# Kernel optimization log

Hardware: AMD Instinct MI355X
Metric: run time of the kernel (lower is better)

## Reference

```python
import jax, jax.numpy as jnp
import numpy as np
from math import sqrt

B = 16
SEQ = 2048          # tokens per sequence (equal-length jagged layout)
L = B * SEQ         # total tokens
D = 512             # embedding dim
P = 8192            # num_position_buckets
NTB = 2048          # num_time_buckets (ts table has NTB+1 rows)
TIME_BUCKET_INCREMENTS = 60.0
TIME_BUCKET_SCALE = 1.0
TIME_DELTA = 0.0
MAX_CONTEXTUAL_SEQ_LEN = 0


def setup_inputs() -> dict:
    key = jax.random.key(0)
    k_emb, k_pos, k_ts, k_time, k_tgt = jax.random.split(key, 5)
    seq_embeddings = jax.random.normal(k_emb, (L, D), dtype=jnp.float32)
    sp = sqrt(1.0 / P)
    pos_weight = jax.random.uniform(k_pos, (P, D), minval=-sp, maxval=sp, dtype=jnp.float32)
    st = sqrt(1.0 / NTB)
    ts_weight = jax.random.uniform(k_ts, (NTB + 1, D), minval=-st, maxval=st, dtype=jnp.float32)
    seq_timestamps = jnp.sort(jax.random.randint(k_time, (L,), 0, 1000000, dtype=jnp.int64) if jax.config.jax_enable_x64 else jax.random.randint(k_time, (L,), 0, 1000000).astype(jnp.int32))
    seq_lengths = jnp.full((B,), SEQ, dtype=jnp.int32)
    seq_offsets = jnp.arange(B + 1, dtype=jnp.int32) * SEQ
    num_targets = jax.random.randint(k_tgt, (B,), 0, 128).astype(jnp.int32)
    return {
        "max_seq_len": SEQ,
        "seq_lengths": seq_lengths,
        "seq_offsets": seq_offsets,
        "seq_embeddings": seq_embeddings,
        "num_targets": num_targets,
        "seq_timestamps": seq_timestamps,
        "pos_weight": pos_weight,
        "ts_weight": ts_weight,
    }


def reference(max_seq_len, seq_lengths, seq_offsets, seq_embeddings,
              num_targets, seq_timestamps, pos_weight, ts_weight):
    total_tokens, dim = seq_embeddings.shape
    batch_size = seq_lengths.shape[0]
    alpha = float(dim) ** 0.5

    # scale residual stream (done before the add in the time-encoding path)
    x = seq_embeddings * alpha

    lengths = seq_offsets[1:] - seq_offsets[:-1]            # [B]
    batch_ids = jnp.repeat(jnp.arange(batch_size, dtype=jnp.int32),
                           lengths, total_repeat_length=total_tokens)  # [L]
    row_ids = jnp.arange(total_tokens, dtype=jnp.int32)
    rel_pos = row_ids - seq_offsets[batch_ids].astype(jnp.int32)        # [L]

    # per-batch high index: seq_len - num_targets (interleave_targets=False)
    high_ind_pb = jnp.maximum(seq_lengths, 0) - jnp.maximum(num_targets, 0)
    high_ind_pb = jnp.maximum(high_ind_pb, 0)
    high_ind = high_ind_pb[batch_ids].astype(jnp.int32)                 # [L]

    max_pos_ind = pos_weight.shape[0]
    pos_ind = jnp.where(rel_pos < high_ind, rel_pos, high_ind)
    pos_ind = high_ind - pos_ind + MAX_CONTEXTUAL_SEQ_LEN
    pos_ind = jnp.minimum(pos_ind, max_pos_ind - 1)
    pos_ind = jnp.where(rel_pos < MAX_CONTEXTUAL_SEQ_LEN, rel_pos, pos_ind)
    pos_ind = jnp.clip(pos_ind, 0, max_pos_ind - 1)

    # timestamp bucket index (time_bucket_fn='sqrt')
    seq_end = seq_offsets[1:]
    query_time_pb = seq_timestamps[seq_end - 1]                         # [B]
    qt = query_time_pb[batch_ids].astype(jnp.float32)
    tt = seq_timestamps.astype(jnp.float32)
    dt = jnp.maximum(qt - tt + TIME_DELTA, 1e-6) / TIME_BUCKET_INCREMENTS
    dt = jnp.sqrt(dt) * TIME_BUCKET_SCALE
    ts_ind = dt.astype(jnp.int32)
    ts_ind = jnp.clip(ts_ind, 0, NTB)
    ts_ind = jnp.minimum(ts_ind, ts_weight.shape[0] - 1)

    # fused gather + add
    return x + (pos_weight[pos_ind] + ts_weight[ts_ind]).astype(x.dtype)
```

## Files before the change

### kernel.cpp

```cpp
#include <hip/hip_runtime.h>
#include <hip/hip_bf16.h>


__global__ __launch_bounds__(256) void hstu_pos_enc_kernel(
    const float4* __restrict__ emb4,
    const float4* __restrict__ posw4,
    const float4* __restrict__ tsw4,
    const int*   __restrict__ seq_offsets,
    const int*   __restrict__ seq_lengths,
    const int*   __restrict__ num_targets,
    const int*   __restrict__ seq_ts,
    float4* __restrict__ out4,
    int L, int D4, int B, int P, int NTB, float alpha)
{
    const int row  = blockIdx.x * 2 + (threadIdx.x >> 7);
    const int lane = threadIdx.x & 127;
    if (row >= L || lane >= D4) return;

    int b = 0;
    while (b + 1 < B && seq_offsets[b + 1] <= row) ++b;

    const int off_b   = seq_offsets[b];
    const int rel_pos = row - off_b;

    int high_ind = max(seq_lengths[b], 0) - max(num_targets[b], 0);
    high_ind = max(high_ind, 0);

    int pos_ind = (rel_pos < high_ind) ? rel_pos : high_ind;
    pos_ind = high_ind - pos_ind;
    pos_ind = min(pos_ind, P - 1);
    pos_ind = max(min(pos_ind, P - 1), 0);

    const float qt = (float)seq_ts[seq_offsets[b + 1] - 1];
    const float tt = (float)seq_ts[row];
    float dt = fmaxf(qt - tt, 1e-6f) * (1.0f / 60.0f);
    dt = sqrtf(dt);
    int ts_ind = (int)dt;
    ts_ind = max(min(ts_ind, NTB), 0);

    const float4 e = emb4[(long)row * D4 + lane];
    const float4 p = posw4[(long)pos_ind * D4 + lane];
    const float4 t = tsw4[(long)ts_ind * D4 + lane];

    float4 o;
    o.x = fmaf(e.x, alpha, p.x + t.x);
    o.y = fmaf(e.y, alpha, p.y + t.y);
    o.z = fmaf(e.z, alpha, p.z + t.z);
    o.w = fmaf(e.w, alpha, p.w + t.w);
    out4[(long)row * D4 + lane] = o;
}

extern "C" void kernel_launch(void* const* d_in, const int* in_sizes, int n_in,
                              void* d_out, int out_size, void* d_ws, size_t ws_size,
                              hipStream_t stream) {
    const int*   seq_lengths = (const int*)d_in[1];
    const int*   seq_offsets = (const int*)d_in[2];
    const float* emb         = (const float*)d_in[3];
    const int*   num_targets = (const int*)d_in[4];
    const int*   seq_ts      = (const int*)d_in[5];
    const float* posw        = (const float*)d_in[6];
    const float* tsw         = (const float*)d_in[7];

    const int B   = in_sizes[1];
    const int L   = in_sizes[5];
    const int D   = in_sizes[3] / L;
    const int D4  = D / 4;
    const int P   = in_sizes[6] / D;
    const int NTB = in_sizes[7] / D - 1;
    const float alpha = sqrtf((float)D);

    const int rows_per_block = 2;
    const int grid = (L + rows_per_block - 1) / rows_per_block;

    hstu_pos_enc_kernel<<<grid, 256, 0, stream>>>(
        (const float4*)emb, (const float4*)posw, (const float4*)tsw,
        seq_offsets, seq_lengths, num_targets, seq_ts,
        (float4*)d_out, L, D4, B, P, NTB, alpha);
}
```

Before: 34.77 us.

## Split index computation into separate kernel and stream gather-add with flat indexing

Per-row index math (batch search, position and time-bucket computation) moves into a small first kernel that writes an int2 per row into the workspace. A second kernel then streams the embedding with flat float4 indexing and gathers the two table rows. This removes the redundant per-thread batch search and timestamp loads, at the cost of an extra launch and a dependent workspace read. The shift-based indexing assumes D4 is a power of two.

```diff
diff --git a/kernel.cpp b/kernel.cpp
--- a/kernel.cpp
+++ b/kernel.cpp
@@ -2,52 +2,69 @@
 #include <hip/hip_bf16.h>
 
 
-__global__ __launch_bounds__(256) void hstu_pos_enc_kernel(
-    const float4* __restrict__ emb4,
-    const float4* __restrict__ posw4,
-    const float4* __restrict__ tsw4,
-    const int*   __restrict__ seq_offsets,
-    const int*   __restrict__ seq_lengths,
-    const int*   __restrict__ num_targets,
-    const int*   __restrict__ seq_ts,
-    float4* __restrict__ out4,
-    int L, int D4, int B, int P, int NTB, float alpha)
+__global__ __launch_bounds__(256) void hstu_idx_kernel(
+    const int* __restrict__ seq_offsets,
+    const int* __restrict__ seq_lengths,
+    const int* __restrict__ num_targets,
+    const int* __restrict__ seq_ts,
+    int2* __restrict__ idx,
+    int L, int B, int P, int NTB)
 {
-    const int row  = blockIdx.x * 2 + (threadIdx.x >> 7);
-    const int lane = threadIdx.x & 127;
-    if (row >= L || lane >= D4) return;
+    __shared__ int soff[257];
+    for (int i = threadIdx.x; i < B + 1 && i < 257; i += blockDim.x)
+        soff[i] = seq_offsets[i];
+    __syncthreads();
+
+    const int row = blockIdx.x * blockDim.x + threadIdx.x;
+    if (row >= L) return;
 
     int b = 0;
-    while (b + 1 < B && seq_offsets[b + 1] <= row) ++b;
+    while (b + 1 < B && soff[b + 1] <= row) ++b;
 
-    const int off_b   = seq_offsets[b];
-    const int rel_pos = row - off_b;
+    const int rel_pos = row - soff[b];
 
     int high_ind = max(seq_lengths[b], 0) - max(num_targets[b], 0);
     high_ind = max(high_ind, 0);
 
     int pos_ind = (rel_pos < high_ind) ? rel_pos : high_ind;
     pos_ind = high_ind - pos_ind;
-    pos_ind = min(pos_ind, P - 1);
     pos_ind = max(min(pos_ind, P - 1), 0);
 
-    const float qt = (float)seq_ts[seq_offsets[b + 1] - 1];
+    const float qt = (float)seq_ts[soff[b + 1] - 1];
     const float tt = (float)seq_ts[row];
     float dt = fmaxf(qt - tt, 1e-6f) * (1.0f / 60.0f);
     dt = sqrtf(dt);
     int ts_ind = (int)dt;
     ts_ind = max(min(ts_ind, NTB), 0);
 
-    const float4 e = emb4[(long)row * D4 + lane];
-    const float4 p = posw4[(long)pos_ind * D4 + lane];
-    const float4 t = tsw4[(long)ts_ind * D4 + lane];
+    idx[row] = make_int2(pos_ind, ts_ind);
+}
+
+__global__ __launch_bounds__(256) void hstu_stream_kernel(
+    const float4* __restrict__ emb4,
+    const float4* __restrict__ posw4,
+    const float4* __restrict__ tsw4,
+    const int2*  __restrict__ idx,
+    float4* __restrict__ out4,
+    long n4, int d4_shift, float alpha)
+{
+    const long gid = (long)blockIdx.x * blockDim.x + threadIdx.x;
+    if (gid >= n4) return;
+
+    const int row  = (int)(gid >> d4_shift);
+    const int lane = (int)gid & ((1 << d4_shift) - 1);
+    const int2 id  = idx[row];
+
+    const float4 e = emb4[gid];
+    const float4 p = posw4[((long)id.x << d4_shift) + lane];
+    const float4 t = tsw4[((long)id.y << d4_shift) + lane];
 
     float4 o;
     o.x = fmaf(e.x, alpha, p.x + t.x);
     o.y = fmaf(e.y, alpha, p.y + t.y);
     o.z = fmaf(e.z, alpha, p.z + t.z);
     o.w = fmaf(e.w, alpha, p.w + t.w);
-    out4[(long)row * D4 + lane] = o;
+    out4[gid] = o;
 }
 
 extern "C" void kernel_launch(void* const* d_in, const int* in_sizes, int n_in,
@@ -69,11 +86,18 @@
     const int NTB = in_sizes[7] / D - 1;
     const float alpha = sqrtf((float)D);
 
-    const int rows_per_block = 2;
-    const int grid = (L + rows_per_block - 1) / rows_per_block;
+    int d4_shift = 0;
+    while ((1 << d4_shift) < D4) ++d4_shift;
 
-    hstu_pos_enc_kernel<<<grid, 256, 0, stream>>>(
+    int2* idx = (int2*)d_ws;
+
+    const int grid_a = (L + 255) / 256;
+    hstu_idx_kernel<<<grid_a, 256, 0, stream>>>(
+        seq_offsets, seq_lengths, num_targets, seq_ts, idx, L, B, P, NTB);
+
+    const long n4 = (long)L * D4;
+    const int grid_b = (int)((n4 + 255) / 256);
+    hstu_stream_kernel<<<grid_b, 256, 0, stream>>>(
         (const float4*)emb, (const float4*)posw, (const float4*)tsw,
-        seq_offsets, seq_lengths, num_targets, seq_ts,
-        (float4*)d_out, L, D4, B, P, NTB, alpha);
+        idx, (float4*)d_out, n4, d4_shift, alpha);
 }
```

New measurement: 36.84 us. 1.06x slower.
